# Performance work log

Hardware: AMD Instinct MI355X
Metric: run time of the kernel (lower is better)

Reference implementation:

```python
import jax, jax.numpy as jnp
import numpy as np

B, L, H, NHEADS = 32, 1024, 128, 2
HEAD = H // NHEADS
NEG = -2.0**32 + 1.0  # padding value used by the torch module


def setup_inputs() -> dict:
    key = jax.random.key(0)
    ks = jax.random.split(key, 9)
    queries = jax.random.normal(ks[0], (B, L, H), dtype=jnp.float32)
    keys = jax.random.normal(ks[1], (B, L, H), dtype=jnp.float32)
    time_mask = jax.random.bernoulli(ks[2], 0.1, (B, L))
    # causal mask: True above the diagonal (future positions masked)
    attn_mask = jnp.triu(jnp.ones((L, L), dtype=bool), k=1)
    s = 1.0 / np.sqrt(H)
    Qw = jax.random.uniform(ks[3], (H, H), jnp.float32, -s, s)
    Qb = jax.random.uniform(ks[4], (H,), jnp.float32, -s, s)
    Kw = jax.random.uniform(ks[5], (H, H), jnp.float32, -s, s)
    Kb = jax.random.uniform(ks[6], (H,), jnp.float32, -s, s)
    Vw = jax.random.uniform(ks[7], (H, H), jnp.float32, -s, s)
    Vb = jax.random.uniform(ks[8], (H,), jnp.float32, -s, s)
    return {"queries": queries, "keys": keys, "time_mask": time_mask,
            "attn_mask": attn_mask, "Qw": Qw, "Qb": Qb, "Kw": Kw, "Kb": Kb,
            "Vw": Vw, "Vb": Vb}


def reference(queries, keys, time_mask, attn_mask, Qw, Qb, Kw, Kb, Vw, Vb):
    b, l, h = queries.shape
    d = h // NHEADS
    # torch Linear: x @ W.T + b
    Q = queries @ Qw.T + Qb
    K = keys @ Kw.T + Kb
    V = keys @ Vw.T + Vb
    # split heads: torch cat(split(dim=2), dim=0) == (h, B, L, d) layout;
    # equivalent per-head math with (B, h, L, d):
    Qh = Q.reshape(b, l, NHEADS, d).transpose(0, 2, 1, 3)  # bhld
    Kh = K.reshape(b, l, NHEADS, d).transpose(0, 2, 1, 3)
    Vh = V.reshape(b, l, NHEADS, d).transpose(0, 2, 1, 3)
    scores = jnp.einsum('bhqd,bhkd->bhqk', Qh, Kh) / jnp.sqrt(
        jnp.asarray(d, dtype=Qh.dtype))
    # time_mask masks whole query rows; attn_mask is causal over (q, k)
    scores = jnp.where(time_mask[:, None, :, None], NEG, scores)
    scores = jnp.where(attn_mask[None, None, :, :], NEG, scores)
    attn = jax.nn.softmax(scores, axis=-1)  # dropout_rate=0 -> identity
    out = jnp.einsum('bhqk,bhkd->bhqd', attn, Vh)
    return out.transpose(0, 2, 1, 3).reshape(b, l, h)
```

## Files before the change

kernel.cpp:

```cpp
#include <hip/hip_runtime.h>

#define LSEQ 1024
#define DH 64
#define NH 2

typedef __attribute__((ext_vector_type(8))) __bf16 bf16x8;
typedef __attribute__((ext_vector_type(4))) float f32x4;
typedef __attribute__((ext_vector_type(16))) float f32x16;
typedef __attribute__((ext_vector_type(4))) unsigned u32x4;
typedef __attribute__((ext_vector_type(8))) unsigned short ushort8;

__device__ __forceinline__ unsigned short f2bf(float f) {
  unsigned u = __float_as_uint(f);
  u += 0x7FFFu + ((u >> 16) & 1u);
  return (unsigned short)(u >> 16);
}
__device__ __forceinline__ unsigned cvt_pk_bf16(float lo, float hi) {
  unsigned r;
  asm("v_cvt_pk_bf16_f32 %0, %1, %2" : "=v"(r) : "v"(lo), "v"(hi));
  return r;
}
__device__ __forceinline__ void gload16(const void* g, void* l) {
  __builtin_amdgcn_global_load_lds(
      (const __attribute__((address_space(1))) void*)g,
      (__attribute__((address_space(3))) void*)l, 16, 0, 0);
}

#define QSCALE 0.1803368801111601f

__global__ __launch_bounds__(256) void wconv_kernel(
    const float* __restrict__ Qw, const float* __restrict__ Kw,
    const float* __restrict__ Vw, unsigned short* __restrict__ Wbf,
    float* __restrict__ Vmean)
{
  for (int i = blockIdx.x * 256 + threadIdx.x; i < NH * 32 * DH; i += 768)
    Vmean[i] = 0.f;
  const float* W = (blockIdx.x == 0) ? Qw : (blockIdx.x == 1) ? Kw : Vw;
  unsigned short* o = Wbf + blockIdx.x * 16384;
  const float4* W4 = (const float4*)W;
#pragma unroll
  for (int i = 0; i < 16; ++i) {
    const int idx = threadIdx.x + i * 256;
    const float4 v = W4[idx];
    uint2 u;
    u.x = cvt_pk_bf16(v.x, v.y);
    u.y = cvt_pk_bf16(v.z, v.w);
    *(uint2*)&o[idx * 4] = u;
  }
}

__global__ __launch_bounds__(256, 2) void proj_kernel(
    const float* __restrict__ queries, const float* __restrict__ keys,
    const unsigned short* __restrict__ Wbf,
    const float* __restrict__ Qb, const float* __restrict__ Kb,
    const float* __restrict__ Vb,
    unsigned short* __restrict__ Qbf, unsigned short* __restrict__ Kbf,
    unsigned short* __restrict__ Vt, float* __restrict__ Vmean)
{
  constexpr int LP = 136;
  __shared__ __align__(16) unsigned short Xs[128 * LP];
  __shared__ __align__(16) unsigned short Ws[16384];

  const int t = threadIdx.x;
  const int lane = t & 63, w = t >> 6;
  const int c = lane & 15, g = lane >> 4;
  const int wrow = w * 32;

  const int mat = blockIdx.x & 1;
  const int rt  = (blockIdx.x >> 1) * 128;

  const float* Xin = mat ? keys : queries;

#define WSTAGE(wi) do {                                                    \
    const char* Wg_ = (const char*)(Wbf + (wi) * 16384);                   \
    _Pragma("unroll")                                                      \
    for (int i_ = 0; i_ < 8; ++i_) {                                       \
      const int off_ = t * 16 + i_ * 4096;                                 \
      const int sch_ = ((((off_ >> 4) & 15) ^ ((off_ >> 8) & 7)) << 4);    \
      gload16(Wg_ + (off_ & ~0xFF) + sch_,                                 \
              (char*)Ws + w * 1024 + i_ * 4096);                           \
    }                                                                      \
  } while (0)

#define WFRAG(ct_, kc_) \
  (*(const bf16x8*)&Ws[((ct_) * 16 + c) * 128 + ((((kc_) * 4 + g) ^ (c & 7)) << 3)])

#define XFRAG(half_, kc_) \
  (*(const bf16x8*)&Xs[(wrow + (half_) * 16 + c) * LP + (kc_) * 32 + g * 8])

  WSTAGE(mat);

  const float4* X4 = (const float4*)(Xin + (size_t)rt * 128);
#pragma unroll
  for (int i = 0; i < 16; ++i) {
    const int e4 = t + i * 256;
    const float4 v = X4[e4];
    const int e = e4 * 4;
    uint2 u;
    u.x = cvt_pk_bf16(v.x, v.y);
    u.y = cvt_pk_bf16(v.z, v.w);
    *(uint2*)&Xs[(e >> 7) * LP + (e & 127)] = u;
  }
  __syncthreads();

  f32x4 accA[2][8];
#pragma unroll
  for (int i = 0; i < 2; ++i)
#pragma unroll
    for (int j = 0; j < 8; ++j) accA[i][j] = (f32x4){0.f, 0.f, 0.f, 0.f};

#pragma unroll
  for (int kc = 0; kc < 4; ++kc) {
    const bf16x8 a0 = XFRAG(0, kc);
    const bf16x8 a1 = XFRAG(1, kc);
#pragma unroll
    for (int ct = 0; ct < 8; ++ct) {
      const bf16x8 bfr = WFRAG(ct, kc);
      accA[0][ct] = __builtin_amdgcn_mfma_f32_16x16x32_bf16(a0, bfr, accA[0][ct], 0, 0, 0);
      accA[1][ct] = __builtin_amdgcn_mfma_f32_16x16x32_bf16(a1, bfr, accA[1][ct], 0, 0, 0);
    }
  }

  f32x4 accB[2][8];
  if (mat) {
    __syncthreads();
    WSTAGE(2);
    __syncthreads();

#pragma unroll
    for (int i = 0; i < 2; ++i)
#pragma unroll
      for (int j = 0; j < 8; ++j) accB[i][j] = (f32x4){0.f, 0.f, 0.f, 0.f};

#pragma unroll
    for (int kc = 0; kc < 4; ++kc) {
      const bf16x8 a0 = XFRAG(0, kc);
      const bf16x8 a1 = XFRAG(1, kc);
#pragma unroll
      for (int ct = 0; ct < 8; ++ct) {
        const bf16x8 bfr = WFRAG(ct, kc);
        accB[0][ct] = __builtin_amdgcn_mfma_f32_16x16x32_bf16(a0, bfr, accB[0][ct], 0, 0, 0);
        accB[1][ct] = __builtin_amdgcn_mfma_f32_16x16x32_bf16(a1, bfr, accB[1][ct], 0, 0, 0);
      }
    }

#pragma unroll
    for (int ct = 0; ct < 8; ++ct) {
      const float bv = Vb[ct * 16 + c];
      float cs = 8.f * bv;
#pragma unroll
      for (int qf = 0; qf < 2; ++qf)
#pragma unroll
        for (int r = 0; r < 4; ++r) cs += accB[qf][ct][r];
      cs += __shfl_xor(cs, 16);
      cs += __shfl_xor(cs, 32);
      if (g == 0) {
        const int col = ct * 16 + c;
        const int bh = (rt >> 10) * NH + (col >> 6);
        atomicAdd(&Vmean[bh * DH + (col & 63)], cs);
      }
    }
  }

  __syncthreads();
  {
    const float* biasA = mat ? Kb : Qb;
    const float qs = mat ? 1.0f : QSCALE;
#pragma unroll
    for (int qf = 0; qf < 2; ++qf)
#pragma unroll
      for (int ct = 0; ct < 8; ++ct) {
        const float bv = biasA[ct * 16 + c];
#pragma unroll
        for (int r = 0; r < 4; ++r)
          Xs[(wrow + qf * 16 + g * 4 + r) * LP + ct * 16 + c] =
              f2bf((accA[qf][ct][r] + bv) * qs);
      }
  }
  __syncthreads();
  {
    unsigned short* outp = (mat ? Kbf : Qbf) + (size_t)rt * 128;
#pragma unroll
    for (int i = 0; i < 8; ++i) {
      const int e = i * 2048 + t * 8;
      *(ushort8*)&outp[e] = *(const ushort8*)&Xs[(e >> 7) * LP + (e & 127)];
    }
  }

  if (mat) {
    __syncthreads();
#pragma unroll
    for (int qf = 0; qf < 2; ++qf)
#pragma unroll
      for (int ct = 0; ct < 8; ++ct) {
        const float bv = Vb[ct * 16 + c];
        const int col = ct * 16 + c;
        uint2 u;
        u.x = cvt_pk_bf16(accB[qf][ct][0] + bv, accB[qf][ct][1] + bv);
        u.y = cvt_pk_bf16(accB[qf][ct][2] + bv, accB[qf][ct][3] + bv);
        *(uint2*)&Xs[col * LP + wrow + qf * 16 + g * 4] = u;
      }
    __syncthreads();
    const int b = rt >> 10, l0 = rt & 1023;
#pragma unroll
    for (int i = 0; i < 8; ++i) {
      const int e = i * 2048 + t * 8;
      const int col = e >> 7, li = e & 127;
      const ushort8 v8 = *(const ushort8*)&Xs[col * LP + li];
      const int hh = col >> 6, dh = col & 63;
      unsigned short* vp = Vt + ((size_t)(b * NH + hh)) * (DH * LSEQ) +
                           (size_t)dh * LSEQ + l0 + li;
      *(ushort8*)vp = v8;
    }
  }
#undef WSTAGE
#undef WFRAG
#undef XFRAG
}

__global__ __launch_bounds__(256, 2) void attn_kernel(
    const unsigned short* __restrict__ Qbf, const unsigned short* __restrict__ Kbf,
    const unsigned short* __restrict__ Vt, const float* __restrict__ Vmean,
    const int* __restrict__ time_mask, float* __restrict__ out)
{
  __shared__ __align__(16) char smem[33280];

  const int tid = threadIdx.x;
  const int lane = tid & 63, w = tid >> 6;
  const int lq = lane & 31, hi = lane >> 5;
  const int s7 = lq & 7;

  const int wgid = blockIdx.x;
  const int xcd = wgid & 7;
  const int idx = wgid >> 3;
  const int bh  = xcd * 8 + (idx & 7);
  const int qb  = 7 - (idx >> 3);
  const int qbase = qb * 128;
  const int b = bh >> 1, h = bh & 1;

  const unsigned short* Qp = Qbf + ((size_t)b * LSEQ) * 128 + h * 64;
  const char* Kpb = (const char*)(Kbf + ((size_t)b * LSEQ) * 128 + h * 64);
  const char* Vpb = (const char*)(Vt + (size_t)bh * (DH * LSEQ));

  const int nkv = qb * 2 + 2;
  const int tkmax = qb * 2 + (w >> 1);

#define STAGE(tkv, bi) do {                                                   \
    const int kv_ = (tkv) * 64;                                               \
    _Pragma("unroll")                                                         \
    for (int r_ = 0; r_ < 2; ++r_) {                                          \
      const int off_ = tid * 16 + r_ * 4096;                                  \
      const int row_ = off_ >> 7;                                             \
      const int chk_ = (((off_ >> 4) & 7) ^ (row_ & 7)) << 4;                 \
      gload16(Kpb + (size_t)(kv_ + row_) * 256 + chk_,                        \
              (char*)smem + (bi) * 8192 + w * 1024 + r_ * 4096);              \
      gload16(Vpb + (size_t)row_ * 2048 + kv_ * 2 + chk_,                     \
              (char*)smem + 16384 + (bi) * 8192 + w * 1024 + r_ * 4096);      \
    }                                                                         \
  } while (0)

#define PLSWAP(x_, y_) asm("v_permlane32_swap_b32 %0, %1" : "+v"(x_), "+v"(y_))

#define MKPA(pk_, m_, dst_) do {                                              \
    unsigned x0_ = pk_[4*(m_)], x1_ = pk_[4*(m_)+1];                          \
    unsigned y0_ = pk_[4*(m_)+2], y1_ = pk_[4*(m_)+3];                        \
    PLSWAP(x0_, y0_); PLSWAP(x1_, y1_);                                       \
    u32x4 u_ = {x0_, x1_, y0_, y1_};                                          \
    dst_ = *(bf16x8*)&u_;                                                     \
  } while (0)

  bf16x8 qa[4];
#pragma unroll
  for (int kc4 = 0; kc4 < 4; ++kc4)
    qa[kc4] = *(const bf16x8*)&Qp[(qbase + w * 32 + lq) * 128 + kc4 * 16 + hi * 8];

  f32x16 acc0 = {}, acc1 = {};
  float lsum = 0.f;

  STAGE(0, 0);
  __syncthreads();

  for (int tk = 0; tk < nkv; ++tk) {
    const int cur = tk & 1;
    if (tk + 1 < nkv) STAGE(tk + 1, cur ^ 1);

    if (tk <= tkmax) {
      const char* Kl = smem + cur * 8192;
      const char* Vl = smem + 16384 + cur * 8192;

      f32x16 s0 = {}, s1 = {};
#pragma unroll
      for (int kc4 = 0; kc4 < 4; ++kc4) {
        const bf16x8 kf = *(const bf16x8*)(Kl + (lq << 7) + (((2 * kc4 + hi) ^ s7) << 4));
        s0 = __builtin_amdgcn_mfma_f32_32x32x16_bf16(kf, qa[kc4], s0, 0, 0, 0);
      }
#pragma unroll
      for (int kc4 = 0; kc4 < 4; ++kc4) {
        const bf16x8 kf = *(const bf16x8*)(Kl + ((32 + lq) << 7) + (((2 * kc4 + hi) ^ s7) << 4));
        s1 = __builtin_amdgcn_mfma_f32_32x32x16_bf16(kf, qa[kc4], s1, 0, 0, 0);
      }

      bf16x8 vf[4][2];
#pragma unroll
      for (int kc4 = 0; kc4 < 4; ++kc4)
#pragma unroll
        for (int dt = 0; dt < 2; ++dt)
          vf[kc4][dt] = *(const bf16x8*)(Vl + ((dt * 32 + lq) << 7) + (((2 * kc4 + hi) ^ s7) << 4));

      const bool diag = (tk == tkmax);
      const int kv = tk * 64;
      const int qrow = qbase + w * 32 + lq;
      float p0[16], p1[16];
#pragma unroll
      for (int r = 0; r < 16; ++r) {
        const int krow = (r & 3) + 8 * (r >> 2) + 4 * hi;
        float e0 = __builtin_amdgcn_exp2f(s0[r]);
        float e1 = __builtin_amdgcn_exp2f(s1[r]);
        if (diag) {
          if (kv + krow > qrow)      e0 = 0.f;
          if (kv + 32 + krow > qrow) e1 = 0.f;
        }
        p0[r] = e0; p1[r] = e1;
        lsum += e0 + e1;
      }

      unsigned pk0[8], pk1[8];
#pragma unroll
      for (int bb = 0; bb < 4; ++bb) {
        pk0[2*bb]   = cvt_pk_bf16(p0[4*bb],   p0[4*bb+1]);
        pk0[2*bb+1] = cvt_pk_bf16(p0[4*bb+2], p0[4*bb+3]);
        pk1[2*bb]   = cvt_pk_bf16(p1[4*bb],   p1[4*bb+1]);
        pk1[2*bb+1] = cvt_pk_bf16(p1[4*bb+2], p1[4*bb+3]);
      }

      bf16x8 pa;
      MKPA(pk0, 0, pa);
      acc0 = __builtin_amdgcn_mfma_f32_32x32x16_bf16(pa, vf[0][0], acc0, 0, 0, 0);
      acc1 = __builtin_amdgcn_mfma_f32_32x32x16_bf16(pa, vf[0][1], acc1, 0, 0, 0);
      MKPA(pk0, 1, pa);
      acc0 = __builtin_amdgcn_mfma_f32_32x32x16_bf16(pa, vf[1][0], acc0, 0, 0, 0);
      acc1 = __builtin_amdgcn_mfma_f32_32x32x16_bf16(pa, vf[1][1], acc1, 0, 0, 0);
      MKPA(pk1, 0, pa);
      acc0 = __builtin_amdgcn_mfma_f32_32x32x16_bf16(pa, vf[2][0], acc0, 0, 0, 0);
      acc1 = __builtin_amdgcn_mfma_f32_32x32x16_bf16(pa, vf[2][1], acc1, 0, 0, 0);
      MKPA(pk1, 1, pa);
      acc0 = __builtin_amdgcn_mfma_f32_32x32x16_bf16(pa, vf[3][0], acc0, 0, 0, 0);
      acc1 = __builtin_amdgcn_mfma_f32_32x32x16_bf16(pa, vf[3][1], acc1, 0, 0, 0);
    }

    __syncthreads();
  }

  float pa_ = lsum, pb_ = lsum;
  PLSWAP(pa_, pb_);
  const float total = lsum + (hi ? pa_ : pb_);

  float* lsx = (float*)(smem + 32768 + w * 128);
  if (hi == 0) {
    const int tm = time_mask[b * LSEQ + qbase + w * 32 + lq];
    lsx[lq] = tm ? -1.0f : 1.0f / total;
  }
  asm volatile("s_waitcnt lgkmcnt(0)" ::: "memory");
  __builtin_amdgcn_sched_barrier(0);

  f32x4 inv4[4];
#pragma unroll
  for (int bb = 0; bb < 4; ++bb)
    inv4[bb] = *(const f32x4*)&lsx[8 * bb + 4 * hi];

  const float vmv0 = Vmean[bh * DH + lq]      * (1.0f / 1024.0f);
  const float vmv1 = Vmean[bh * DH + 32 + lq] * (1.0f / 1024.0f);

#pragma unroll
  for (int r = 0; r < 16; ++r) {
    const int qr = (r & 3) + 8 * (r >> 2) + 4 * hi;
    const float wv = inv4[r >> 2][r & 3];
    float* orow = out + (size_t)(b * LSEQ + qbase + w * 32 + qr) * (NH * DH) + h * DH;
    orow[lq]      = (wv < 0.f) ? vmv0 : acc0[r] * wv;
    orow[32 + lq] = (wv < 0.f) ? vmv1 : acc1[r] * wv;
  }
#undef STAGE
#undef PLSWAP
#undef MKPA
}

extern "C" void kernel_launch(void* const* d_in, const int* in_sizes, int n_in,
                              void* d_out, int out_size, void* d_ws, size_t ws_size,
                              hipStream_t stream) {
  const float* queries   = (const float*)d_in[0];
  const float* keys      = (const float*)d_in[1];
  const int*   time_mask = (const int*)d_in[2];
  const float* Qw = (const float*)d_in[4];
  const float* Qb = (const float*)d_in[5];
  const float* Kw = (const float*)d_in[6];
  const float* Kb = (const float*)d_in[7];
  const float* Vw = (const float*)d_in[8];
  const float* Vb = (const float*)d_in[9];
  float* out = (float*)d_out;

  char* ws = (char*)d_ws;
  unsigned short* Wbf   = (unsigned short*)(ws);
  float*          Vmean = (float*)(ws + 98304);
  unsigned short* Qbf   = (unsigned short*)(ws + 114688);
  unsigned short* Kbf   = (unsigned short*)(ws + 8503296);
  unsigned short* Vtp   = (unsigned short*)(ws + 16891904);

  wconv_kernel<<<3, 256, 0, stream>>>(Qw, Kw, Vw, Wbf, Vmean);
  proj_kernel<<<512, 256, 0, stream>>>(queries, keys, Wbf, Qb, Kb, Vb,
                                       Qbf, Kbf, Vtp, Vmean);
  attn_kernel<<<512, 256, 0, stream>>>(Qbf, Kbf, Vtp, Vmean, time_mask, out);
}
```

Before: 49.90 us.

## Halve projection tiles, read weights from global, compute row sums via MFMA, add setprio

The weight-conversion kernel now runs across 48 blocks with one float4 per thread instead of 3 blocks looping. The projection kernel uses 64-row tiles over 1024 blocks and reads weight fragments directly from global/L2 instead of staging them in LDS, which shrinks LDS use and permits higher occupancy. The attention kernel replaces the scalar softmax row-sum and its cross-lane exchange with an extra MFMA against a ones vector, and wraps the MFMA bursts in s_setprio. The extra MFMA adds matrix work and the global weight reads may cost more latency.

Result: slower. 84.23 us (+68.8%).

```diff
diff --git a/kernel.cpp b/kernel.cpp
--- a/kernel.cpp
+++ b/kernel.cpp
@@ -33,23 +33,18 @@
     const float* __restrict__ Vw, unsigned short* __restrict__ Wbf,
     float* __restrict__ Vmean)
 {
-  for (int i = blockIdx.x * 256 + threadIdx.x; i < NH * 32 * DH; i += 768)
-    Vmean[i] = 0.f;
-  const float* W = (blockIdx.x == 0) ? Qw : (blockIdx.x == 1) ? Kw : Vw;
-  unsigned short* o = Wbf + blockIdx.x * 16384;
-  const float4* W4 = (const float4*)W;
-#pragma unroll
-  for (int i = 0; i < 16; ++i) {
-    const int idx = threadIdx.x + i * 256;
-    const float4 v = W4[idx];
-    uint2 u;
-    u.x = cvt_pk_bf16(v.x, v.y);
-    u.y = cvt_pk_bf16(v.z, v.w);
-    *(uint2*)&o[idx * 4] = u;
-  }
-}
-
-__global__ __launch_bounds__(256, 2) void proj_kernel(
+  const int t = blockIdx.x * 256 + threadIdx.x;
+  if (t < NH * 32 * DH) Vmean[t] = 0.f;
+  const int m = t >> 12;
+  const float* W = (m == 0) ? Qw : (m == 1) ? Kw : Vw;
+  const float4 v = ((const float4*)W)[t & 4095];
+  uint2 u;
+  u.x = cvt_pk_bf16(v.x, v.y);
+  u.y = cvt_pk_bf16(v.z, v.w);
+  *(uint2*)&Wbf[t * 4] = u;
+}
+
+__global__ __launch_bounds__(256, 3) void proj_kernel(
     const float* __restrict__ queries, const float* __restrict__ keys,
     const unsigned short* __restrict__ Wbf,
     const float* __restrict__ Qb, const float* __restrict__ Kb,
@@ -58,41 +53,20 @@
     unsigned short* __restrict__ Vt, float* __restrict__ Vmean)
 {
   constexpr int LP = 136;
-  __shared__ __align__(16) unsigned short Xs[128 * LP];
-  __shared__ __align__(16) unsigned short Ws[16384];
+  constexpr int TP = 72;
+  __shared__ __align__(16) unsigned short Xs[9216];
 
   const int t = threadIdx.x;
   const int lane = t & 63, w = t >> 6;
   const int c = lane & 15, g = lane >> 4;
-  const int wrow = w * 32;
 
   const int mat = blockIdx.x & 1;
-  const int rt  = (blockIdx.x >> 1) * 128;
-
+  const int rt  = (blockIdx.x >> 1) * 64;
   const float* Xin = mat ? keys : queries;
 
-#define WSTAGE(wi) do {                                                    \
-    const char* Wg_ = (const char*)(Wbf + (wi) * 16384);                   \
-    _Pragma("unroll")                                                      \
-    for (int i_ = 0; i_ < 8; ++i_) {                                       \
-      const int off_ = t * 16 + i_ * 4096;                                 \
-      const int sch_ = ((((off_ >> 4) & 15) ^ ((off_ >> 8) & 7)) << 4);    \
-      gload16(Wg_ + (off_ & ~0xFF) + sch_,                                 \
-              (char*)Ws + w * 1024 + i_ * 4096);                           \
-    }                                                                      \
-  } while (0)
-
-#define WFRAG(ct_, kc_) \
-  (*(const bf16x8*)&Ws[((ct_) * 16 + c) * 128 + ((((kc_) * 4 + g) ^ (c & 7)) << 3)])
-
-#define XFRAG(half_, kc_) \
-  (*(const bf16x8*)&Xs[(wrow + (half_) * 16 + c) * LP + (kc_) * 32 + g * 8])
-
-  WSTAGE(mat);
-
   const float4* X4 = (const float4*)(Xin + (size_t)rt * 128);
 #pragma unroll
-  for (int i = 0; i < 16; ++i) {
+  for (int i = 0; i < 8; ++i) {
     const int e4 = t + i * 256;
     const float4 v = X4[e4];
     const int e = e4 * 4;
@@ -103,55 +77,46 @@
   }
   __syncthreads();
 
-  f32x4 accA[2][8];
-#pragma unroll
-  for (int i = 0; i < 2; ++i)
-#pragma unroll
-    for (int j = 0; j < 8; ++j) accA[i][j] = (f32x4){0.f, 0.f, 0.f, 0.f};
+  const unsigned short* WA = Wbf + mat * 16384;
+  f32x4 accA[8];
+#pragma unroll
+  for (int j = 0; j < 8; ++j) accA[j] = (f32x4){0.f, 0.f, 0.f, 0.f};
 
 #pragma unroll
   for (int kc = 0; kc < 4; ++kc) {
-    const bf16x8 a0 = XFRAG(0, kc);
-    const bf16x8 a1 = XFRAG(1, kc);
-#pragma unroll
-    for (int ct = 0; ct < 8; ++ct) {
-      const bf16x8 bfr = WFRAG(ct, kc);
-      accA[0][ct] = __builtin_amdgcn_mfma_f32_16x16x32_bf16(a0, bfr, accA[0][ct], 0, 0, 0);
-      accA[1][ct] = __builtin_amdgcn_mfma_f32_16x16x32_bf16(a1, bfr, accA[1][ct], 0, 0, 0);
-    }
-  }
-
-  f32x4 accB[2][8];
+    bf16x8 wf[8];
+#pragma unroll
+    for (int ct = 0; ct < 8; ++ct)
+      wf[ct] = *(const bf16x8*)&WA[(ct * 16 + c) * 128 + kc * 32 + g * 8];
+    const bf16x8 a = *(const bf16x8*)&Xs[(w * 16 + c) * LP + kc * 32 + g * 8];
+#pragma unroll
+    for (int ct = 0; ct < 8; ++ct)
+      accA[ct] = __builtin_amdgcn_mfma_f32_16x16x32_bf16(a, wf[ct], accA[ct], 0, 0, 0);
+  }
+
+  f32x4 accB[8];
   if (mat) {
-    __syncthreads();
-    WSTAGE(2);
-    __syncthreads();
-
-#pragma unroll
-    for (int i = 0; i < 2; ++i)
-#pragma unroll
-      for (int j = 0; j < 8; ++j) accB[i][j] = (f32x4){0.f, 0.f, 0.f, 0.f};
-
+    const unsigned short* WB = Wbf + 2 * 16384;
+#pragma unroll
+    for (int j = 0; j < 8; ++j) accB[j] = (f32x4){0.f, 0.f, 0.f, 0.f};
 #pragma unroll
     for (int kc = 0; kc < 4; ++kc) {
-      const bf16x8 a0 = XFRAG(0, kc);
-      const bf16x8 a1 = XFRAG(1, kc);
-#pragma unroll
-      for (int ct = 0; ct < 8; ++ct) {
-        const bf16x8 bfr = WFRAG(ct, kc);
-        accB[0][ct] = __builtin_amdgcn_mfma_f32_16x16x32_bf16(a0, bfr, accB[0][ct], 0, 0, 0);
-        accB[1][ct] = __builtin_amdgcn_mfma_f32_16x16x32_bf16(a1, bfr, accB[1][ct], 0, 0, 0);
-      }
+      bf16x8 wf[8];
+#pragma unroll
+      for (int ct = 0; ct < 8; ++ct)
+        wf[ct] = *(const bf16x8*)&WB[(ct * 16 + c) * 128 + kc * 32 + g * 8];
+      const bf16x8 a = *(const bf16x8*)&Xs[(w * 16 + c) * LP + kc * 32 + g * 8];
+#pragma unroll
+      for (int ct = 0; ct < 8; ++ct)
+        accB[ct] = __builtin_amdgcn_mfma_f32_16x16x32_bf16(a, wf[ct], accB[ct], 0, 0, 0);
     }
 
 #pragma unroll
     for (int ct = 0; ct < 8; ++ct) {
       const float bv = Vb[ct * 16 + c];
-      float cs = 8.f * bv;
-#pragma unroll
-      for (int qf = 0; qf < 2; ++qf)
-#pragma unroll
-        for (int r = 0; r < 4; ++r) cs += accB[qf][ct][r];
+      float cs = 4.f * bv;
+#pragma unroll
+      for (int r = 0; r < 4; ++r) cs += accB[ct][r];
       cs += __shfl_xor(cs, 16);
       cs += __shfl_xor(cs, 32);
       if (g == 0) {
@@ -167,21 +132,18 @@
     const float* biasA = mat ? Kb : Qb;
     const float qs = mat ? 1.0f : QSCALE;
 #pragma unroll
-    for (int qf = 0; qf < 2; ++qf)
-#pragma unroll
-      for (int ct = 0; ct < 8; ++ct) {
-        const float bv = biasA[ct * 16 + c];
-#pragma unroll
-        for (int r = 0; r < 4; ++r)
-          Xs[(wrow + qf * 16 + g * 4 + r) * LP + ct * 16 + c] =
-              f2bf((accA[qf][ct][r] + bv) * qs);
-      }
+    for (int ct = 0; ct < 8; ++ct) {
+      const float bv = biasA[ct * 16 + c];
+#pragma unroll
+      for (int r = 0; r < 4; ++r)
+        Xs[(w * 16 + g * 4 + r) * LP + ct * 16 + c] = f2bf((accA[ct][r] + bv) * qs);
+    }
   }
   __syncthreads();
   {
     unsigned short* outp = (mat ? Kbf : Qbf) + (size_t)rt * 128;
 #pragma unroll
-    for (int i = 0; i < 8; ++i) {
+    for (int i = 0; i < 4; ++i) {
       const int e = i * 2048 + t * 8;
       *(ushort8*)&outp[e] = *(const ushort8*)&Xs[(e >> 7) * LP + (e & 127)];
     }
@@ -190,32 +152,27 @@
   if (mat) {
     __syncthreads();
 #pragma unroll
-    for (int qf = 0; qf < 2; ++qf)
-#pragma unroll
-      for (int ct = 0; ct < 8; ++ct) {
-        const float bv = Vb[ct * 16 + c];
-        const int col = ct * 16 + c;
-        uint2 u;
-        u.x = cvt_pk_bf16(accB[qf][ct][0] + bv, accB[qf][ct][1] + bv);
-        u.y = cvt_pk_bf16(accB[qf][ct][2] + bv, accB[qf][ct][3] + bv);
-        *(uint2*)&Xs[col * LP + wrow + qf * 16 + g * 4] = u;
-      }
+    for (int ct = 0; ct < 8; ++ct) {
+      const float bv = Vb[ct * 16 + c];
+      const int col = ct * 16 + c;
+      uint2 u;
+      u.x = cvt_pk_bf16(accB[ct][0] + bv, accB[ct][1] + bv);
+      u.y = cvt_pk_bf16(accB[ct][2] + bv, accB[ct][3] + bv);
+      *(uint2*)&Xs[col * TP + w * 16 + g * 4] = u;
+    }
     __syncthreads();
     const int b = rt >> 10, l0 = rt & 1023;
 #pragma unroll
-    for (int i = 0; i < 8; ++i) {
+    for (int i = 0; i < 4; ++i) {
       const int e = i * 2048 + t * 8;
-      const int col = e >> 7, li = e & 127;
-      const ushort8 v8 = *(const ushort8*)&Xs[col * LP + li];
+      const int col = e >> 6, li = e & 63;
+      const ushort8 v8 = *(const ushort8*)&Xs[col * TP + li];
       const int hh = col >> 6, dh = col & 63;
       unsigned short* vp = Vt + ((size_t)(b * NH + hh)) * (DH * LSEQ) +
                            (size_t)dh * LSEQ + l0 + li;
       *(ushort8*)vp = v8;
     }
   }
-#undef WSTAGE
-#undef WFRAG
-#undef XFRAG
 }
 
 __global__ __launch_bounds__(256, 2) void attn_kernel(
@@ -274,8 +231,10 @@
   for (int kc4 = 0; kc4 < 4; ++kc4)
     qa[kc4] = *(const bf16x8*)&Qp[(qbase + w * 32 + lq) * 128 + kc4 * 16 + hi * 8];
 
-  f32x16 acc0 = {}, acc1 = {};
-  float lsum = 0.f;
+  const __bf16 one = (__bf16)1.0f;
+  const bf16x8 vones = {one, one, one, one, one, one, one, one};
+
+  f32x16 acc0 = {}, acc1 = {}, acc5 = {};
 
   STAGE(0, 0);
   __syncthreads();
@@ -289,6 +248,7 @@
       const char* Vl = smem + 16384 + cur * 8192;
 
       f32x16 s0 = {}, s1 = {};
+      __builtin_amdgcn_s_setprio(1);
 #pragma unroll
       for (int kc4 = 0; kc4 < 4; ++kc4) {
         const bf16x8 kf = *(const bf16x8*)(Kl + (lq << 7) + (((2 * kc4 + hi) ^ s7) << 4));
@@ -299,6 +259,7 @@
         const bf16x8 kf = *(const bf16x8*)(Kl + ((32 + lq) << 7) + (((2 * kc4 + hi) ^ s7) << 4));
         s1 = __builtin_amdgcn_mfma_f32_32x32x16_bf16(kf, qa[kc4], s1, 0, 0, 0);
       }
+      __builtin_amdgcn_s_setprio(0);
 
       bf16x8 vf[4][2];
 #pragma unroll
@@ -321,7 +282,6 @@
           if (kv + 32 + krow > qrow) e1 = 0.f;
         }
         p0[r] = e0; p1[r] = e1;
-        lsum += e0 + e1;
       }
 
       unsigned pk0[8], pk1[8];
@@ -334,50 +294,46 @@
       }
 
       bf16x8 pa;
+      __builtin_amdgcn_s_setprio(1);
       MKPA(pk0, 0, pa);
       acc0 = __builtin_amdgcn_mfma_f32_32x32x16_bf16(pa, vf[0][0], acc0, 0, 0, 0);
       acc1 = __builtin_amdgcn_mfma_f32_32x32x16_bf16(pa, vf[0][1], acc1, 0, 0, 0);
+      acc5 = __builtin_amdgcn_mfma_f32_32x32x16_bf16(pa, vones,    acc5, 0, 0, 0);
       MKPA(pk0, 1, pa);
       acc0 = __builtin_amdgcn_mfma_f32_32x32x16_bf16(pa, vf[1][0], acc0, 0, 0, 0);
       acc1 = __builtin_amdgcn_mfma_f32_32x32x16_bf16(pa, vf[1][1], acc1, 0, 0, 0);
+      acc5 = __builtin_amdgcn_mfma_f32_32x32x16_bf16(pa, vones,    acc5, 0, 0, 0);
       MKPA(pk1, 0, pa);
       acc0 = __builtin_amdgcn_mfma_f32_32x32x16_bf16(pa, vf[2][0], acc0, 0, 0, 0);
       acc1 = __builtin_amdgcn_mfma_f32_32x32x16_bf16(pa, vf[2][1], acc1, 0, 0, 0);
+      acc5 = __builtin_amdgcn_mfma_f32_32x32x16_bf16(pa, vones,    acc5, 0, 0, 0);
       MKPA(pk1, 1, pa);
       acc0 = __builtin_amdgcn_mfma_f32_32x32x16_bf16(pa, vf[3][0], acc0, 0, 0, 0);
       acc1 = __builtin_amdgcn_mfma_f32_32x32x16_bf16(pa, vf[3][1], acc1, 0, 0, 0);
+      acc5 = __builtin_amdgcn_mfma_f32_32x32x16_bf16(pa, vones,    acc5, 0, 0, 0);
+      __builtin_amdgcn_s_setprio(0);
     }
 
     __syncthreads();
   }
 
-  float pa_ = lsum, pb_ = lsum;
-  PLSWAP(pa_, pb_);
-  const float total = lsum + (hi ? pa_ : pb_);
-
-  float* lsx = (float*)(smem + 32768 + w * 128);
-  if (hi == 0) {
-    const int tm = time_mask[b * LSEQ + qbase + w * 32 + lq];
-    lsx[lq] = tm ? -1.0f : 1.0f / total;
-  }
+  int* tmx = (int*)(smem + 32768 + w * 128);
+  if (hi == 0)
+    tmx[lq] = time_mask[b * LSEQ + qbase + w * 32 + lq];
   asm volatile("s_waitcnt lgkmcnt(0)" ::: "memory");
   __builtin_amdgcn_sched_barrier(0);
 
-  f32x4 inv4[4];
-#pragma unroll
-  for (int bb = 0; bb < 4; ++bb)
-    inv4[bb] = *(const f32x4*)&lsx[8 * bb + 4 * hi];
-
   const float vmv0 = Vmean[bh * DH + lq]      * (1.0f / 1024.0f);
   const float vmv1 = Vmean[bh * DH + 32 + lq] * (1.0f / 1024.0f);
 
 #pragma unroll
   for (int r = 0; r < 16; ++r) {
     const int qr = (r & 3) + 8 * (r >> 2) + 4 * hi;
-    const float wv = inv4[r >> 2][r & 3];
+    const int tm = tmx[qr];
+    const float wv = 1.0f / acc5[r];
     float* orow = out + (size_t)(b * LSEQ + qbase + w * 32 + qr) * (NH * DH) + h * DH;
-    orow[lq]      = (wv < 0.f) ? vmv0 : acc0[r] * wv;
-    orow[32 + lq] = (wv < 0.f) ? vmv1 : acc1[r] * wv;
+    orow[lq]      = tm ? vmv0 : acc0[r] * wv;
+    orow[32 + lq] = tm ? vmv1 : acc1[r] * wv;
   }
 #undef STAGE
 #undef PLSWAP
@@ -405,8 +361,8 @@
   unsigned short* Kbf   = (unsigned short*)(ws + 8503296);
   unsigned short* Vtp   = (unsigned short*)(ws + 16891904);
 
-  wconv_kernel<<<3, 256, 0, stream>>>(Qw, Kw, Vw, Wbf, Vmean);
-  proj_kernel<<<512, 256, 0, stream>>>(queries, keys, Wbf, Qb, Kb, Vb,
-                                       Qbf, Kbf, Vtp, Vmean);
+  wconv_kernel<<<48, 256, 0, stream>>>(Qw, Kw, Vw, Wbf, Vmean);
+  proj_kernel<<<1024, 256, 0, stream>>>(queries, keys, Wbf, Qb, Kb, Vb,
+                                        Qbf, Kbf, Vtp, Vmean);
   attn_kernel<<<512, 256, 0, stream>>>(Qbf, Kbf, Vtp, Vmean, time_mask, out);
 }
```

## Split attention into 64-row query tiles and compute row sums via MFMA

Applied to the files above, without the earlier changes.

The attention kernel now uses 128-thread blocks over 64-row query tiles, doubling the grid to 1024 blocks. This removes the per-wave causal skip imbalance, since the two waves share every KV tile. The softmax denominator is now taken from an extra MFMA against a ones vector instead of scalar adds plus a cross-lane swap. The MFMA sections are wrapped in s_setprio. Weight conversion is spread over 48 blocks instead of 3 to parallelise that small kernel. In exchange, each KV tile staged to shared memory is reused by only two waves instead of four, and there are more MFMA instructions per tile.

Result: faster. 47.97 us (median of 2 runs) (-3.9%).

```diff
diff --git a/kernel.cpp b/kernel.cpp
--- a/kernel.cpp
+++ b/kernel.cpp
@@ -33,20 +33,15 @@
     const float* __restrict__ Vw, unsigned short* __restrict__ Wbf,
     float* __restrict__ Vmean)
 {
-  for (int i = blockIdx.x * 256 + threadIdx.x; i < NH * 32 * DH; i += 768)
-    Vmean[i] = 0.f;
-  const float* W = (blockIdx.x == 0) ? Qw : (blockIdx.x == 1) ? Kw : Vw;
-  unsigned short* o = Wbf + blockIdx.x * 16384;
-  const float4* W4 = (const float4*)W;
-#pragma unroll
-  for (int i = 0; i < 16; ++i) {
-    const int idx = threadIdx.x + i * 256;
-    const float4 v = W4[idx];
-    uint2 u;
-    u.x = cvt_pk_bf16(v.x, v.y);
-    u.y = cvt_pk_bf16(v.z, v.w);
-    *(uint2*)&o[idx * 4] = u;
-  }
+  const int t = blockIdx.x * 256 + threadIdx.x;
+  if (t < NH * 32 * DH) Vmean[t] = 0.f;
+  const int m = t >> 12;
+  const float* W = (m == 0) ? Qw : (m == 1) ? Kw : Vw;
+  const float4 v = ((const float4*)W)[t & 4095];
+  uint2 u;
+  u.x = cvt_pk_bf16(v.x, v.y);
+  u.y = cvt_pk_bf16(v.z, v.w);
+  *(uint2*)&Wbf[t * 4] = u;
 }
 
 __global__ __launch_bounds__(256, 2) void proj_kernel(
@@ -68,7 +63,6 @@
 
   const int mat = blockIdx.x & 1;
   const int rt  = (blockIdx.x >> 1) * 128;
-
   const float* Xin = mat ? keys : queries;
 
 #define WSTAGE(wi) do {                                                    \
@@ -218,7 +212,7 @@
 #undef XFRAG
 }
 
-__global__ __launch_bounds__(256, 2) void attn_kernel(
+__global__ __launch_bounds__(128, 2) void attn_kernel(
     const unsigned short* __restrict__ Qbf, const unsigned short* __restrict__ Kbf,
     const unsigned short* __restrict__ Vt, const float* __restrict__ Vmean,
     const int* __restrict__ time_mask, float* __restrict__ out)
@@ -234,28 +228,27 @@
   const int xcd = wgid & 7;
   const int idx = wgid >> 3;
   const int bh  = xcd * 8 + (idx & 7);
-  const int qb  = 7 - (idx >> 3);
-  const int qbase = qb * 128;
+  const int qt  = 15 - (idx >> 3);
+  const int qbase = qt * 64;
   const int b = bh >> 1, h = bh & 1;
 
   const unsigned short* Qp = Qbf + ((size_t)b * LSEQ) * 128 + h * 64;
   const char* Kpb = (const char*)(Kbf + ((size_t)b * LSEQ) * 128 + h * 64);
   const char* Vpb = (const char*)(Vt + (size_t)bh * (DH * LSEQ));
 
-  const int nkv = qb * 2 + 2;
-  const int tkmax = qb * 2 + (w >> 1);
+  const int nkv = qt + 1;
 
 #define STAGE(tkv, bi) do {                                                   \
     const int kv_ = (tkv) * 64;                                               \
     _Pragma("unroll")                                                         \
-    for (int r_ = 0; r_ < 2; ++r_) {                                          \
-      const int off_ = tid * 16 + r_ * 4096;                                  \
+    for (int r_ = 0; r_ < 4; ++r_) {                                          \
+      const int off_ = tid * 16 + r_ * 2048;                                  \
       const int row_ = off_ >> 7;                                             \
       const int chk_ = (((off_ >> 4) & 7) ^ (row_ & 7)) << 4;                 \
       gload16(Kpb + (size_t)(kv_ + row_) * 256 + chk_,                        \
-              (char*)smem + (bi) * 8192 + w * 1024 + r_ * 4096);              \
+              (char*)smem + (bi) * 8192 + r_ * 2048 + tid * 16);              \
       gload16(Vpb + (size_t)row_ * 2048 + kv_ * 2 + chk_,                     \
-              (char*)smem + 16384 + (bi) * 8192 + w * 1024 + r_ * 4096);      \
+              (char*)smem + 16384 + (bi) * 8192 + r_ * 2048 + tid * 16);      \
     }                                                                         \
   } while (0)
 
@@ -274,8 +267,10 @@
   for (int kc4 = 0; kc4 < 4; ++kc4)
     qa[kc4] = *(const bf16x8*)&Qp[(qbase + w * 32 + lq) * 128 + kc4 * 16 + hi * 8];
 
-  f32x16 acc0 = {}, acc1 = {};
-  float lsum = 0.f;
+  const __bf16 one = (__bf16)1.0f;
+  const bf16x8 vones = {one, one, one, one, one, one, one, one};
+
+  f32x16 acc0 = {}, acc1 = {}, acc5 = {};
 
   STAGE(0, 0);
   __syncthreads();
@@ -284,100 +279,95 @@
     const int cur = tk & 1;
     if (tk + 1 < nkv) STAGE(tk + 1, cur ^ 1);
 
-    if (tk <= tkmax) {
-      const char* Kl = smem + cur * 8192;
-      const char* Vl = smem + 16384 + cur * 8192;
-
-      f32x16 s0 = {}, s1 = {};
-#pragma unroll
-      for (int kc4 = 0; kc4 < 4; ++kc4) {
-        const bf16x8 kf = *(const bf16x8*)(Kl + (lq << 7) + (((2 * kc4 + hi) ^ s7) << 4));
-        s0 = __builtin_amdgcn_mfma_f32_32x32x16_bf16(kf, qa[kc4], s0, 0, 0, 0);
+    const char* Kl = smem + cur * 8192;
+    const char* Vl = smem + 16384 + cur * 8192;
+
+    f32x16 s0 = {}, s1 = {};
+    __builtin_amdgcn_s_setprio(1);
+#pragma unroll
+    for (int kc4 = 0; kc4 < 4; ++kc4) {
+      const bf16x8 kf = *(const bf16x8*)(Kl + (lq << 7) + (((2 * kc4 + hi) ^ s7) << 4));
+      s0 = __builtin_amdgcn_mfma_f32_32x32x16_bf16(kf, qa[kc4], s0, 0, 0, 0);
+    }
+#pragma unroll
+    for (int kc4 = 0; kc4 < 4; ++kc4) {
+      const bf16x8 kf = *(const bf16x8*)(Kl + ((32 + lq) << 7) + (((2 * kc4 + hi) ^ s7) << 4));
+      s1 = __builtin_amdgcn_mfma_f32_32x32x16_bf16(kf, qa[kc4], s1, 0, 0, 0);
+    }
+    __builtin_amdgcn_s_setprio(0);
+
+    bf16x8 vf[4][2];
+#pragma unroll
+    for (int kc4 = 0; kc4 < 4; ++kc4)
+#pragma unroll
+      for (int dt = 0; dt < 2; ++dt)
+        vf[kc4][dt] = *(const bf16x8*)(Vl + ((dt * 32 + lq) << 7) + (((2 * kc4 + hi) ^ s7) << 4));
+
+    const bool diag = (tk == nkv - 1);
+    const int kv = tk * 64;
+    const int qrow = qbase + w * 32 + lq;
+    float p0[16], p1[16];
+#pragma unroll
+    for (int r = 0; r < 16; ++r) {
+      const int krow = (r & 3) + 8 * (r >> 2) + 4 * hi;
+      float e0 = __builtin_amdgcn_exp2f(s0[r]);
+      float e1 = __builtin_amdgcn_exp2f(s1[r]);
+      if (diag) {
+        if (kv + krow > qrow)      e0 = 0.f;
+        if (kv + 32 + krow > qrow) e1 = 0.f;
       }
-#pragma unroll
-      for (int kc4 = 0; kc4 < 4; ++kc4) {
-        const bf16x8 kf = *(const bf16x8*)(Kl + ((32 + lq) << 7) + (((2 * kc4 + hi) ^ s7) << 4));
-        s1 = __builtin_amdgcn_mfma_f32_32x32x16_bf16(kf, qa[kc4], s1, 0, 0, 0);
-      }
-
-      bf16x8 vf[4][2];
-#pragma unroll
-      for (int kc4 = 0; kc4 < 4; ++kc4)
-#pragma unroll
-        for (int dt = 0; dt < 2; ++dt)
-          vf[kc4][dt] = *(const bf16x8*)(Vl + ((dt * 32 + lq) << 7) + (((2 * kc4 + hi) ^ s7) << 4));
-
-      const bool diag = (tk == tkmax);
-      const int kv = tk * 64;
-      const int qrow = qbase + w * 32 + lq;
-      float p0[16], p1[16];
-#pragma unroll
-      for (int r = 0; r < 16; ++r) {
-        const int krow = (r & 3) + 8 * (r >> 2) + 4 * hi;
-        float e0 = __builtin_amdgcn_exp2f(s0[r]);
-        float e1 = __builtin_amdgcn_exp2f(s1[r]);
-        if (diag) {
-          if (kv + krow > qrow)      e0 = 0.f;
-          if (kv + 32 + krow > qrow) e1 = 0.f;
-        }
-        p0[r] = e0; p1[r] = e1;
-        lsum += e0 + e1;
-      }
-
-      unsigned pk0[8], pk1[8];
-#pragma unroll
-      for (int bb = 0; bb < 4; ++bb) {
-        pk0[2*bb]   = cvt_pk_bf16(p0[4*bb],   p0[4*bb+1]);
-        pk0[2*bb+1] = cvt_pk_bf16(p0[4*bb+2], p0[4*bb+3]);
-        pk1[2*bb]   = cvt_pk_bf16(p1[4*bb],   p1[4*bb+1]);
-        pk1[2*bb+1] = cvt_pk_bf16(p1[4*bb+2], p1[4*bb+3]);
-      }
-
-      bf16x8 pa;
-      MKPA(pk0, 0, pa);
-      acc0 = __builtin_amdgcn_mfma_f32_32x32x16_bf16(pa, vf[0][0], acc0, 0, 0, 0);
-      acc1 = __builtin_amdgcn_mfma_f32_32x32x16_bf16(pa, vf[0][1], acc1, 0, 0, 0);
-      MKPA(pk0, 1, pa);
-      acc0 = __builtin_amdgcn_mfma_f32_32x32x16_bf16(pa, vf[1][0], acc0, 0, 0, 0);
-      acc1 = __builtin_amdgcn_mfma_f32_32x32x16_bf16(pa, vf[1][1], acc1, 0, 0, 0);
-      MKPA(pk1, 0, pa);
-      acc0 = __builtin_amdgcn_mfma_f32_32x32x16_bf16(pa, vf[2][0], acc0, 0, 0, 0);
-      acc1 = __builtin_amdgcn_mfma_f32_32x32x16_bf16(pa, vf[2][1], acc1, 0, 0, 0);
-      MKPA(pk1, 1, pa);
-      acc0 = __builtin_amdgcn_mfma_f32_32x32x16_bf16(pa, vf[3][0], acc0, 0, 0, 0);
-      acc1 = __builtin_amdgcn_mfma_f32_32x32x16_bf16(pa, vf[3][1], acc1, 0, 0, 0);
-    }
+      p0[r] = e0; p1[r] = e1;
+    }
+
+    unsigned pk0[8], pk1[8];
+#pragma unroll
+    for (int bb = 0; bb < 4; ++bb) {
+      pk0[2*bb]   = cvt_pk_bf16(p0[4*bb],   p0[4*bb+1]);
+      pk0[2*bb+1] = cvt_pk_bf16(p0[4*bb+2], p0[4*bb+3]);
+      pk1[2*bb]   = cvt_pk_bf16(p1[4*bb],   p1[4*bb+1]);
+      pk1[2*bb+1] = cvt_pk_bf16(p1[4*bb+2], p1[4*bb+3]);
+    }
+
+    bf16x8 pa;
+    __builtin_amdgcn_s_setprio(1);
+    MKPA(pk0, 0, pa);
+    acc0 = __builtin_amdgcn_mfma_f32_32x32x16_bf16(pa, vf[0][0], acc0, 0, 0, 0);
+    acc1 = __builtin_amdgcn_mfma_f32_32x32x16_bf16(pa, vf[0][1], acc1, 0, 0, 0);
+    acc5 = __builtin_amdgcn_mfma_f32_32x32x16_bf16(pa, vones,    acc5, 0, 0, 0);
+    MKPA(pk0, 1, pa);
+    acc0 = __builtin_amdgcn_mfma_f32_32x32x16_bf16(pa, vf[1][0], acc0, 0, 0, 0);
+    acc1 = __builtin_amdgcn_mfma_f32_32x32x16_bf16(pa, vf[1][1], acc1, 0, 0, 0);
+    acc5 = __builtin_amdgcn_mfma_f32_32x32x16_bf16(pa, vones,    acc5, 0, 0, 0);
+    MKPA(pk1, 0, pa);
+    acc0 = __builtin_amdgcn_mfma_f32_32x32x16_bf16(pa, vf[2][0], acc0, 0, 0, 0);
+    acc1 = __builtin_amdgcn_mfma_f32_32x32x16_bf16(pa, vf[2][1], acc1, 0, 0, 0);
+    acc5 = __builtin_amdgcn_mfma_f32_32x32x16_bf16(pa, vones,    acc5, 0, 0, 0);
+    MKPA(pk1, 1, pa);
+    acc0 = __builtin_amdgcn_mfma_f32_32x32x16_bf16(pa, vf[3][0], acc0, 0, 0, 0);
+    acc1 = __builtin_amdgcn_mfma_f32_32x32x16_bf16(pa, vf[3][1], acc1, 0, 0, 0);
+    acc5 = __builtin_amdgcn_mfma_f32_32x32x16_bf16(pa, vones,    acc5, 0, 0, 0);
+    __builtin_amdgcn_s_setprio(0);
 
     __syncthreads();
   }
 
-  float pa_ = lsum, pb_ = lsum;
-  PLSWAP(pa_, pb_);
-  const float total = lsum + (hi ? pa_ : pb_);
-
-  float* lsx = (float*)(smem + 32768 + w * 128);
-  if (hi == 0) {
-    const int tm = time_mask[b * LSEQ + qbase + w * 32 + lq];
-    lsx[lq] = tm ? -1.0f : 1.0f / total;
-  }
+  int* tmx = (int*)(smem + 32768 + w * 128);
+  if (hi == 0)
+    tmx[lq] = time_mask[b * LSEQ + qbase + w * 32 + lq];
   asm volatile("s_waitcnt lgkmcnt(0)" ::: "memory");
   __builtin_amdgcn_sched_barrier(0);
 
-  f32x4 inv4[4];
-#pragma unroll
-  for (int bb = 0; bb < 4; ++bb)
-    inv4[bb] = *(const f32x4*)&lsx[8 * bb + 4 * hi];
-
   const float vmv0 = Vmean[bh * DH + lq]      * (1.0f / 1024.0f);
   const float vmv1 = Vmean[bh * DH + 32 + lq] * (1.0f / 1024.0f);
 
 #pragma unroll
   for (int r = 0; r < 16; ++r) {
     const int qr = (r & 3) + 8 * (r >> 2) + 4 * hi;
-    const float wv = inv4[r >> 2][r & 3];
+    const int tm = tmx[qr];
+    const float wv = 1.0f / acc5[r];
     float* orow = out + (size_t)(b * LSEQ + qbase + w * 32 + qr) * (NH * DH) + h * DH;
-    orow[lq]      = (wv < 0.f) ? vmv0 : acc0[r] * wv;
-    orow[32 + lq] = (wv < 0.f) ? vmv1 : acc1[r] * wv;
+    orow[lq]      = tm ? vmv0 : acc0[r] * wv;
+    orow[32 + lq] = tm ? vmv1 : acc1[r] * wv;
   }
 #undef STAGE
 #undef PLSWAP
@@ -405,8 +395,8 @@
   unsigned short* Kbf   = (unsigned short*)(ws + 8503296);
   unsigned short* Vtp   = (unsigned short*)(ws + 16891904);
 
-  wconv_kernel<<<3, 256, 0, stream>>>(Qw, Kw, Vw, Wbf, Vmean);
+  wconv_kernel<<<48, 256, 0, stream>>>(Qw, Kw, Vw, Wbf, Vmean);
   proj_kernel<<<512, 256, 0, stream>>>(queries, keys, Wbf, Qb, Kb, Vb,
                                        Qbf, Kbf, Vtp, Vmean);
-  attn_kernel<<<512, 256, 0, stream>>>(Qbf, Kbf, Vtp, Vmean, time_mask, out);
-}
+  attn_kernel<<<1024, 128, 0, stream>>>(Qbf, Kbf, Vtp, Vmean, time_mask, out);
+}
```

## Widen weight conversion grid, batch input loads, raise attention occupancy, add MFMA priority

Applied to the files above, without the earlier changes.

The weight-conversion kernel now runs on 48 blocks with one float4 per thread instead of 3 blocks looping 16 times, so that tiny prologue kernel has less latency. The projection kernel issues all 16 input loads before converting them, using an asm barrier so the loads stay in flight together. The attention kernel asks for 3 waves per SIMD through launch bounds, raises wave priority around its MFMA blocks, and simplifies the LDS destination offsets used for staging. The higher occupancy target may force register spills, and the extra load registers in projection may cut its occupancy.

Result: no change. 49.99 us (+0.2%).

```diff
diff --git a/kernel.cpp b/kernel.cpp
--- a/kernel.cpp
+++ b/kernel.cpp
@@ -33,20 +33,15 @@
     const float* __restrict__ Vw, unsigned short* __restrict__ Wbf,
     float* __restrict__ Vmean)
 {
-  for (int i = blockIdx.x * 256 + threadIdx.x; i < NH * 32 * DH; i += 768)
-    Vmean[i] = 0.f;
-  const float* W = (blockIdx.x == 0) ? Qw : (blockIdx.x == 1) ? Kw : Vw;
-  unsigned short* o = Wbf + blockIdx.x * 16384;
-  const float4* W4 = (const float4*)W;
-#pragma unroll
-  for (int i = 0; i < 16; ++i) {
-    const int idx = threadIdx.x + i * 256;
-    const float4 v = W4[idx];
-    uint2 u;
-    u.x = cvt_pk_bf16(v.x, v.y);
-    u.y = cvt_pk_bf16(v.z, v.w);
-    *(uint2*)&o[idx * 4] = u;
-  }
+  const int t = blockIdx.x * 256 + threadIdx.x;
+  if (t < NH * 32 * DH) Vmean[t] = 0.f;
+  const int m = t >> 12;
+  const float* W = (m == 0) ? Qw : (m == 1) ? Kw : Vw;
+  const float4 v = ((const float4*)W)[t & 4095];
+  uint2 u;
+  u.x = cvt_pk_bf16(v.x, v.y);
+  u.y = cvt_pk_bf16(v.z, v.w);
+  *(uint2*)&Wbf[t * 4] = u;
 }
 
 __global__ __launch_bounds__(256, 2) void proj_kernel(
@@ -68,7 +63,6 @@
 
   const int mat = blockIdx.x & 1;
   const int rt  = (blockIdx.x >> 1) * 128;
-
   const float* Xin = mat ? keys : queries;
 
 #define WSTAGE(wi) do {                                                    \
@@ -91,14 +85,18 @@
   WSTAGE(mat);
 
   const float4* X4 = (const float4*)(Xin + (size_t)rt * 128);
+  float4 xv[16];
+#pragma unroll
+  for (int i = 0; i < 16; ++i) xv[i] = X4[t + i * 256];
+#pragma unroll
+  for (int i = 0; i < 16; ++i)
+    asm volatile("" : "+v"(xv[i].x), "+v"(xv[i].y), "+v"(xv[i].z), "+v"(xv[i].w));
 #pragma unroll
   for (int i = 0; i < 16; ++i) {
-    const int e4 = t + i * 256;
-    const float4 v = X4[e4];
-    const int e = e4 * 4;
+    const int e = (t + i * 256) * 4;
     uint2 u;
-    u.x = cvt_pk_bf16(v.x, v.y);
-    u.y = cvt_pk_bf16(v.z, v.w);
+    u.x = cvt_pk_bf16(xv[i].x, xv[i].y);
+    u.y = cvt_pk_bf16(xv[i].z, xv[i].w);
     *(uint2*)&Xs[(e >> 7) * LP + (e & 127)] = u;
   }
   __syncthreads();
@@ -218,7 +216,7 @@
 #undef XFRAG
 }
 
-__global__ __launch_bounds__(256, 2) void attn_kernel(
+__global__ __launch_bounds__(256, 3) void attn_kernel(
     const unsigned short* __restrict__ Qbf, const unsigned short* __restrict__ Kbf,
     const unsigned short* __restrict__ Vt, const float* __restrict__ Vmean,
     const int* __restrict__ time_mask, float* __restrict__ out)
@@ -242,8 +240,8 @@
   const char* Kpb = (const char*)(Kbf + ((size_t)b * LSEQ) * 128 + h * 64);
   const char* Vpb = (const char*)(Vt + (size_t)bh * (DH * LSEQ));
 
-  const int nkv = qb * 2 + 2;
-  const int tkmax = qb * 2 + (w >> 1);
+  const int nkv = 2 * qb + 2;
+  const int tkmax = 2 * qb + (w >> 1);
 
 #define STAGE(tkv, bi) do {                                                   \
     const int kv_ = (tkv) * 64;                                               \
@@ -253,9 +251,9 @@
       const int row_ = off_ >> 7;                                             \
       const int chk_ = (((off_ >> 4) & 7) ^ (row_ & 7)) << 4;                 \
       gload16(Kpb + (size_t)(kv_ + row_) * 256 + chk_,                        \
-              (char*)smem + (bi) * 8192 + w * 1024 + r_ * 4096);              \
+              (char*)smem + (bi) * 8192 + off_);                              \
       gload16(Vpb + (size_t)row_ * 2048 + kv_ * 2 + chk_,                     \
-              (char*)smem + 16384 + (bi) * 8192 + w * 1024 + r_ * 4096);      \
+              (char*)smem + 16384 + (bi) * 8192 + off_);                      \
     }                                                                         \
   } while (0)
 
@@ -289,6 +287,7 @@
       const char* Vl = smem + 16384 + cur * 8192;
 
       f32x16 s0 = {}, s1 = {};
+      __builtin_amdgcn_s_setprio(1);
 #pragma unroll
       for (int kc4 = 0; kc4 < 4; ++kc4) {
         const bf16x8 kf = *(const bf16x8*)(Kl + (lq << 7) + (((2 * kc4 + hi) ^ s7) << 4));
@@ -299,6 +298,7 @@
         const bf16x8 kf = *(const bf16x8*)(Kl + ((32 + lq) << 7) + (((2 * kc4 + hi) ^ s7) << 4));
         s1 = __builtin_amdgcn_mfma_f32_32x32x16_bf16(kf, qa[kc4], s1, 0, 0, 0);
       }
+      __builtin_amdgcn_s_setprio(0);
 
       bf16x8 vf[4][2];
 #pragma unroll
@@ -334,6 +334,7 @@
       }
 
       bf16x8 pa;
+      __builtin_amdgcn_s_setprio(1);
       MKPA(pk0, 0, pa);
       acc0 = __builtin_amdgcn_mfma_f32_32x32x16_bf16(pa, vf[0][0], acc0, 0, 0, 0);
       acc1 = __builtin_amdgcn_mfma_f32_32x32x16_bf16(pa, vf[0][1], acc1, 0, 0, 0);
@@ -346,6 +347,7 @@
       MKPA(pk1, 1, pa);
       acc0 = __builtin_amdgcn_mfma_f32_32x32x16_bf16(pa, vf[3][0], acc0, 0, 0, 0);
       acc1 = __builtin_amdgcn_mfma_f32_32x32x16_bf16(pa, vf[3][1], acc1, 0, 0, 0);
+      __builtin_amdgcn_s_setprio(0);
     }
 
     __syncthreads();
@@ -405,7 +407,7 @@
   unsigned short* Kbf   = (unsigned short*)(ws + 8503296);
   unsigned short* Vtp   = (unsigned short*)(ws + 16891904);
 
-  wconv_kernel<<<3, 256, 0, stream>>>(Qw, Kw, Vw, Wbf, Vmean);
+  wconv_kernel<<<48, 256, 0, stream>>>(Qw, Kw, Vw, Wbf, Vmean);
   proj_kernel<<<512, 256, 0, stream>>>(queries, keys, Wbf, Qb, Kb, Vb,
                                        Qbf, Kbf, Vtp, Vmean);
   attn_kernel<<<512, 256, 0, stream>>>(Qbf, Kbf, Vtp, Vmean, time_mask, out);
```
